# Optimization experiments

Measured on AMD Instinct MI355X. Metric: run time of the kernel, lower is better.

## Reference

```python
import jax, jax.numpy as jnp
import numpy as np

K = 8
D_IN = 300 + K   # 308
H = 100          # hidden size hardcoded throughout the module
N = 768          # num_words (words in one table)


def setup_inputs() -> dict:
    key = jax.random.key(0)
    ks = jax.random.split(key, 24)
    f32 = jnp.float32

    def rn(k, shape, scale=0.05):
        return jax.random.normal(k, shape, dtype=f32) * scale

    inp = {
        'vv': jax.random.normal(ks[0], (N, D_IN), dtype=f32),
        'indices': jax.random.randint(ks[1], (N, 5), 0, N),
        'indices_not_found': jax.random.randint(ks[2], (N,), 0, 2).astype(bool),
        'num_words': N,
        # ModuleA: Linear(308, 100) + tanh
        'A_W': rn(ks[3], (D_IN, H)), 'A_b': jnp.zeros((H,), f32),
        # ModuleB: consumes concat(ww[N,500], hh[N,100]) -> Linear(600,100)+tanh
        'B_W': rn(ks[4], (5 * H + H, H)), 'B_b': jnp.zeros((H,), f32),
        # ModuleB2(100,100,100): two heads, oo and new hidden hh
        'B2_Wo': rn(ks[5], (H, H)), 'B2_bo': jnp.zeros((H,), f32),
        'B2_Wh': rn(ks[6], (H, H)), 'B2_bh': jnp.zeros((H,), f32),
        # ModuleD(100,100)
        'D_W': rn(ks[7], (H, H)), 'D_b': jnp.zeros((H,), f32),
    }
    # Three ModuleAssociate2 heads (rows/cols/cells): pairwise 2-layer MLP
    # score(o_i, o_j) = Linear(H,2)(relu(Linear(2H,H)(concat(o_i,o_j))))
    for i, name in enumerate(['rows', 'cols', 'cells']):
        k1, k2 = jax.random.split(ks[8 + i])
        inp[name + '_W1'] = rn(k1, (2 * H, H))
        inp[name + '_b1'] = jnp.zeros((H,), f32)
        inp[name + '_W2'] = rn(k2, (H, 2))
        inp[name + '_b2'] = jnp.zeros((2,), f32)
    return inp


def _concat_neighbors(uu, indices, not_found):
    # gather 5 neighbor feature rows -> (N, 5*H); zero rows where not found
    y = uu[indices].reshape(indices.shape[0], 5 * uu.shape[1])  # (N,5,H)->(N,500)
    return jnp.where(not_found[:, None], 0.0, y)


def _associate(o, W1, b1, W2, b2):
    # pairwise MLP over all (i,j) pairs without materializing the 2H concat:
    # concat(o_i,o_j) @ W1 == o_i @ W1[:H] + o_j @ W1[H:]
    h = o.shape[1]
    hl = o @ W1[:h]   # (N,H)
    hr = o @ W1[h:]   # (N,H)
    hid = jax.nn.relu(hl[:, None, :] + hr[None, :, :] + b1)  # (N,N,H)
    return hid @ W2 + b2  # (N,N,2)


def reference(indices, indices_not_found, vv, num_words,
              A_W, A_b, B_W, B_b, B2_Wo, B2_bo, B2_Wh, B2_bh, D_W, D_b,
              rows_W1, rows_b1, rows_W2, rows_b2,
              cols_W1, cols_b1, cols_W2, cols_b2,
              cells_W1, cells_b1, cells_W2, cells_b2):
    iterations = 1
    uu = jnp.tanh(vv @ A_W + A_b)                 # ModuleA: (N,100)
    hh = jnp.zeros((num_words, H), vv.dtype)
    for _ in range(iterations):
        ww = _concat_neighbors(uu, indices, indices_not_found)  # (N,500)
        bb = jnp.tanh(jnp.concatenate([ww, hh], axis=1) @ B_W + B_b)  # ModuleB
        oo = jnp.tanh(bb @ B2_Wo + B2_bo)          # ModuleB2 output head
        hh = jnp.tanh(bb @ B2_Wh + B2_bh)          # ModuleB2 hidden head
        uu = jnp.tanh(hh @ D_W + D_b)              # ModuleD
    return (_associate(oo, rows_W1, rows_b1, rows_W2, rows_b2),
            _associate(oo, cols_W1, cols_b1, cols_W2, cols_b2),
            _associate(oo, cells_W1, cells_b1, cells_W2, cells_b2))
```

## Files before the change

### kernel.cpp

```cpp
#include <hip/hip_runtime.h>
#include <hip/hip_bf16.h>

#define NW   768
#define HID  100
#define DIN  308
#define RPB  2
#define TJ   64

typedef const float* fp;

__global__ __launch_bounds__(512) void k_uu(fp vv, fp A_W, fp A_b,
                                            float* __restrict__ uu) {
    __shared__ float vs[RPB][DIN];
    __shared__ float part[4][RPB][128];
    const int i0 = blockIdx.x * RPB;
    for (int t = threadIdx.x; t < RPB * DIN; t += 512) {
        const int r = t / DIN, k = t % DIN;
        vs[r][k] = vv[(i0 + r) * DIN + k];
    }
    __syncthreads();
    const int c = threadIdx.x & 127;
    const int s = threadIdx.x >> 7;
    float a0 = 0.f, a1 = 0.f;
    if (c < HID) {
        const int k0 = s * 77;
#pragma unroll 11
        for (int k = k0; k < k0 + 77; ++k) {
            const float w = A_W[k * HID + c];
            a0 = fmaf(vs[0][k], w, a0);
            a1 = fmaf(vs[1][k], w, a1);
        }
    }
    part[s][0][c] = a0; part[s][1][c] = a1;
    __syncthreads();
    for (int t = threadIdx.x; t < RPB * HID; t += 512) {
        const int r = t / HID, cc = t % HID;
        float acc = A_b[cc];
#pragma unroll
        for (int s2 = 0; s2 < 4; ++s2) acc += part[s2][r][cc];
        uu[(i0 + r) * HID + cc] = tanhf(acc);
    }
}

__global__ __launch_bounds__(640) void k_fused(
    const float* __restrict__ uu, const int* __restrict__ indices,
    const int* __restrict__ nf,
    fp B_W, fp B_b, fp B2_Wo, fp B2_bo,
    fp W1r, fp b1r, fp W1c, fp b1c, fp W1e, fp b1e,
    float* __restrict__ hlhr) {
    __shared__ __align__(16) float ww[RPB][5 * HID];
    __shared__ float part[5][RPB][128];
    __shared__ __align__(16) float bbs[RPB][HID];
    __shared__ __align__(16) float oos[RPB][HID];
    __shared__ int flags[6];
    __shared__ int smode[2];

    if (threadIdx.x < 6) flags[threadIdx.x] = 0;
    __syncthreads();
    if (threadIdx.x < 192) {
        const int t = threadIdx.x;
        const unsigned vn = (unsigned)nf[t];
        if (vn > 1u) atomicOr(&flags[0], 1);
        if (vn & 0xFEFEFEFEu) atomicOr(&flags[1], 1);
        if ((t & 1) && vn) atomicOr(&flags[2], 1);
        if (!(t & 1) && vn) atomicOr(&flags[3], 1);
        const unsigned vi = (unsigned)indices[t];
        if ((t & 1) && vi) atomicOr(&flags[4], 1);
        if (!(t & 1) && vi) atomicOr(&flags[5], 1);
    }
    __syncthreads();
    if (threadIdx.x == 0) {
        int m = 0;
        if (!flags[1] && flags[0]) m = 1;
        else if (!flags[2] && flags[3]) m = 2;
        smode[0] = m;
        smode[1] = (!flags[4] && flags[5]) ? 1 : 0;
    }
    __syncthreads();
    const int mnf = smode[0], midx = smode[1];

    const int i0 = blockIdx.x * RPB;
    for (int t = threadIdx.x; t < RPB * 5 * HID; t += 640) {
        const int r = t / (5 * HID), u = t % (5 * HID);
        const int i = i0 + r;
        const bool notf = (mnf == 1) ? (((const unsigned char*)nf)[i] != 0)
                        : (mnf == 2) ? (nf[2 * i] != 0)
                                     : (nf[i] != 0);
        const int q = u / HID, cc = u % HID;
        int j = midx ? indices[2 * (i * 5 + q)] : indices[i * 5 + q];
        j = (j < 0) ? 0 : ((j >= NW) ? NW - 1 : j);
        ww[r][u] = notf ? 0.f : uu[j * HID + cc];
    }
    __syncthreads();

    const int c = threadIdx.x % 128;
    const int s = threadIdx.x / 128;

    {
        float a0 = 0.f, a1 = 0.f;
        if (c < HID) {
            const int k0 = s * 100;
#pragma unroll 5
            for (int k = k0; k < k0 + 100; k += 4) {
                const float4 w0 = *(const float4*)&ww[0][k];
                const float4 w1 = *(const float4*)&ww[1][k];
                const float b0 = B_W[(k + 0) * HID + c];
                const float b1v = B_W[(k + 1) * HID + c];
                const float b2v = B_W[(k + 2) * HID + c];
                const float b3 = B_W[(k + 3) * HID + c];
                a0 = fmaf(w0.x, b0, a0); a1 = fmaf(w1.x, b0, a1);
                a0 = fmaf(w0.y, b1v, a0); a1 = fmaf(w1.y, b1v, a1);
                a0 = fmaf(w0.z, b2v, a0); a1 = fmaf(w1.z, b2v, a1);
                a0 = fmaf(w0.w, b3, a0); a1 = fmaf(w1.w, b3, a1);
            }
        }
        part[s][0][c] = a0; part[s][1][c] = a1;
    }
    __syncthreads();
    for (int t = threadIdx.x; t < RPB * HID; t += 640) {
        const int r = t / HID, cc = t % HID;
        float acc = B_b[cc];
#pragma unroll
        for (int s2 = 0; s2 < 5; ++s2) acc += part[s2][r][cc];
        bbs[r][cc] = tanhf(acc);
    }
    __syncthreads();

    {
        float a0 = 0.f, a1 = 0.f;
        if (c < HID) {
            const int k0 = s * 20;
#pragma unroll 5
            for (int k = k0; k < k0 + 20; k += 4) {
                const float4 w0 = *(const float4*)&bbs[0][k];
                const float4 w1 = *(const float4*)&bbs[1][k];
                const float b0 = B2_Wo[(k + 0) * HID + c];
                const float b1v = B2_Wo[(k + 1) * HID + c];
                const float b2v = B2_Wo[(k + 2) * HID + c];
                const float b3 = B2_Wo[(k + 3) * HID + c];
                a0 = fmaf(w0.x, b0, a0); a1 = fmaf(w1.x, b0, a1);
                a0 = fmaf(w0.y, b1v, a0); a1 = fmaf(w1.y, b1v, a1);
                a0 = fmaf(w0.z, b2v, a0); a1 = fmaf(w1.z, b2v, a1);
                a0 = fmaf(w0.w, b3, a0); a1 = fmaf(w1.w, b3, a1);
            }
        }
        part[s][0][c] = a0; part[s][1][c] = a1;
    }
    __syncthreads();
    for (int t = threadIdx.x; t < RPB * HID; t += 640) {
        const int r = t / HID, cc = t % HID;
        float acc = B2_bo[cc];
#pragma unroll
        for (int s2 = 0; s2 < 5; ++s2) acc += part[s2][r][cc];
        oos[r][cc] = tanhf(acc);
    }
    __syncthreads();

    const int u = threadIdx.x;
    if (u < 600) {
        const int ho = u / HID;
        const int cc = u % HID;
        const int h = ho >> 1, half = ho & 1;
        fp W1 = (h == 0) ? W1r : ((h == 1) ? W1c : W1e);
        fp b1 = (h == 0) ? b1r : ((h == 1) ? b1c : b1e);
        const float bias = half ? 0.f : b1[cc];
        float a0 = bias, a1 = bias;
        const float* Wp = W1 + half * HID * HID;
#pragma unroll 5
        for (int k = 0; k < HID; k += 4) {
            const float4 o0 = *(const float4*)&oos[0][k];
            const float4 o1 = *(const float4*)&oos[1][k];
            const float b0 = Wp[(k + 0) * HID + cc];
            const float b1v = Wp[(k + 1) * HID + cc];
            const float b2v = Wp[(k + 2) * HID + cc];
            const float b3 = Wp[(k + 3) * HID + cc];
            a0 = fmaf(o0.x, b0, a0); a1 = fmaf(o1.x, b0, a1);
            a0 = fmaf(o0.y, b1v, a0); a1 = fmaf(o1.y, b1v, a1);
            a0 = fmaf(o0.z, b2v, a0); a1 = fmaf(o1.z, b2v, a1);
            a0 = fmaf(o0.w, b3, a0); a1 = fmaf(o1.w, b3, a1);
        }
        hlhr[(size_t)ho * (NW * HID) + (size_t)(i0 + 0) * HID + cc] = a0;
        hlhr[(size_t)ho * (NW * HID) + (size_t)(i0 + 1) * HID + cc] = a1;
    }
}

__global__ __launch_bounds__(256) void k_pair(
    const float* __restrict__ hlhr,
    fp W2r, fp b2r, fp W2c, fp b2c, fp W2e, fp b2e,
    float* __restrict__ out) {
    __shared__ __align__(16) float hlS[HID][TJ];
    __shared__ __align__(16) float hrS[HID][TJ];
    __shared__ __align__(16) float2 w2s[HID];

    const int h  = blockIdx.z;
    const int i0 = blockIdx.y * TJ;
    const int j0 = blockIdx.x * TJ;
    const float* hl = hlhr + (size_t)(h * 2 + 0) * (NW * HID) + (size_t)i0 * HID;
    const float* hr = hlhr + (size_t)(h * 2 + 1) * (NW * HID) + (size_t)j0 * HID;

    for (int t = threadIdx.x; t < TJ * HID; t += 256) {
        const int r = t / HID, k = t % HID;
        const int rs = r ^ ((k & 7) << 2);
        hlS[k][rs] = hl[t];
        hrS[k][rs] = hr[t];
    }
    fp W2 = (h == 0) ? W2r : ((h == 1) ? W2c : W2e);
    fp b2 = (h == 0) ? b2r : ((h == 1) ? b2c : b2e);
    if (threadIdx.x < HID) {
        w2s[threadIdx.x] = make_float2(W2[2 * threadIdx.x], W2[2 * threadIdx.x + 1]);
    }
    __syncthreads();

    const int tx = threadIdx.x & 15;
    const int ty = threadIdx.x >> 4;
    float2 acc[4][4];
#pragma unroll
    for (int ii = 0; ii < 4; ++ii)
#pragma unroll
        for (int jj = 0; jj < 4; ++jj) acc[ii][jj] = make_float2(0.f, 0.f);

    for (int k = 0; k < HID; ++k) {
        const int sw = (k & 7) << 2;
        const float4 a4 = *(const float4*)&hlS[k][(ty * 4) ^ sw];
        const float4 r4 = *(const float4*)&hrS[k][(tx * 4) ^ sw];
        const float2 w2 = w2s[k];
        const float av[4] = {a4.x, a4.y, a4.z, a4.w};
        const float rv[4] = {r4.x, r4.y, r4.z, r4.w};
#pragma unroll
        for (int ii = 0; ii < 4; ++ii)
#pragma unroll
            for (int jj = 0; jj < 4; ++jj) {
                const float hv = fmaxf(av[ii] + rv[jj], 0.f);
                acc[ii][jj].x = fmaf(hv, w2.x, acc[ii][jj].x);
                acc[ii][jj].y = fmaf(hv, w2.y, acc[ii][jj].y);
            }
    }

    const float b20 = b2[0];
    const float b21 = b2[1];
#pragma unroll
    for (int ii = 0; ii < 4; ++ii) {
        const int i = i0 + ty * 4 + ii;
        const size_t rowo = ((size_t)(h * NW + i) * NW + j0 + tx * 4) * 2;
        float4 v0, v1;
        v0.x = acc[ii][0].x + b20; v0.y = acc[ii][0].y + b21;
        v0.z = acc[ii][1].x + b20; v0.w = acc[ii][1].y + b21;
        v1.x = acc[ii][2].x + b20; v1.y = acc[ii][2].y + b21;
        v1.z = acc[ii][3].x + b20; v1.w = acc[ii][3].y + b21;
        *reinterpret_cast<float4*>(out + rowo)     = v0;
        *reinterpret_cast<float4*>(out + rowo + 4) = v1;
    }
}

extern "C" void kernel_launch(void* const* d_in, const int* in_sizes, int n_in,
                              void* d_out, int out_size, void* d_ws,
                              size_t ws_size, hipStream_t stream) {
    int i_vv = -1, i_idx = -1, i_nf = -1, i_AW = -1, i_BW = -1;
    int tens[3] = {-1, -1, -1}; int n10 = 0;
    int w1s[3]  = {-1, -1, -1}; int n20 = 0;
    int w2s_[3] = {-1, -1, -1}; int n200 = 0;
    int b100[8] = {-1, -1, -1, -1, -1, -1, -1, -1}; int nb = 0;
    int b2s[3]  = {-1, -1, -1}; int nb2 = 0;
    for (int i = 0; i < n_in; ++i) {
        switch (in_sizes[i]) {
            case 236544: i_vv = i; break;
            case 3840:   i_idx = i; break;
            case 768:    i_nf = i; break;
            case 30800:  i_AW = i; break;
            case 60000:  i_BW = i; break;
            case 10000:  if (n10 < 3) tens[n10++] = i; break;
            case 20000:  if (n20 < 3) w1s[n20++] = i; break;
            case 200:    if (n200 < 3) w2s_[n200++] = i; break;
            case 100:    if (nb < 8) b100[nb++] = i; break;
            case 2:      if (nb2 < 3) b2s[nb2++] = i; break;
            default: break;
        }
    }
    fp vv          = (fp)d_in[i_vv];
    const int* idx = (const int*)d_in[i_idx];
    const int* nf  = (const int*)d_in[i_nf];
    fp A_W = (fp)d_in[i_AW],      A_b   = (fp)d_in[b100[0]];
    fp B_W = (fp)d_in[i_BW],      B_b   = (fp)d_in[b100[1]];
    fp B2_Wo = (fp)d_in[tens[0]], B2_bo = (fp)d_in[b100[2]];
    fp W1r = (fp)d_in[w1s[0]], b1r = (fp)d_in[b100[5]];
    fp W1c = (fp)d_in[w1s[1]], b1c = (fp)d_in[b100[6]];
    fp W1e = (fp)d_in[w1s[2]], b1e = (fp)d_in[b100[7]];
    fp W2r = (fp)d_in[w2s_[0]], b2r = (fp)d_in[b2s[0]];
    fp W2c = (fp)d_in[w2s_[1]], b2c = (fp)d_in[b2s[1]];
    fp W2e = (fp)d_in[w2s_[2]], b2e = (fp)d_in[b2s[2]];

    float* out = (float*)d_out;

    float* ws   = (float*)d_ws;
    float* uu   = ws;
    float* hlhr = ws + NW * HID;

    k_uu<<<NW / RPB, 512, 0, stream>>>(vv, A_W, A_b, uu);
    k_fused<<<NW / RPB, 640, 0, stream>>>(uu, idx, nf, B_W, B_b,
                                          B2_Wo, B2_bo,
                                          W1r, b1r, W1c, b1c, W1e, b1e, hlhr);
    dim3 grid(NW / TJ, NW / TJ, 3);
    k_pair<<<grid, 256, 0, stream>>>(hlhr, W2r, b2r, W2c, b2c, W2e, b2e, out);
}
```

Measured before the change: 55.23 us.

## Transpose hl/hr to k-major layout before pairwise kernel, drop LDS swizzle

Adds a transpose kernel that rewrites the hl/hr projections into a feature-major [H][N] layout, so the pairwise kernel can load its shared tiles with coalesced, unswizzled row copies. The pairwise kernel also drops the shared W2 staging and reads the W2 weights directly from global memory (uniform loads), splits the accumulators into two arrays, and unrolls the k loop by 4. This adds an extra kernel launch plus a round trip of the 6x768x100 buffer through memory. Without the XOR swizzle, the float4 shared reads may now hit more bank conflicts.

```diff
diff --git a/kernel.cpp b/kernel.cpp
--- a/kernel.cpp
+++ b/kernel.cpp
@@ -184,46 +184,58 @@
     }
 }
 
+__global__ __launch_bounds__(256) void k_tr(const float* __restrict__ in,
+                                            float* __restrict__ outT) {
+    __shared__ float ld[64 * 101];
+    const int ho = blockIdx.y;
+    const int i0 = blockIdx.x * 64;
+    const float* src = in + (size_t)ho * (NW * HID) + (size_t)i0 * HID;
+    float* dst = outT + (size_t)ho * (HID * NW);
+    for (int t = threadIdx.x; t < 64 * HID; t += 256) {
+        const int r = t / HID, c = t % HID;
+        ld[r * 101 + c] = src[t];
+    }
+    __syncthreads();
+    for (int t = threadIdx.x; t < 64 * HID; t += 256) {
+        const int k = t >> 6, r = t & 63;
+        dst[(size_t)k * NW + i0 + r] = ld[r * 101 + k];
+    }
+}
+
 __global__ __launch_bounds__(256) void k_pair(
-    const float* __restrict__ hlhr,
+    const float* __restrict__ hlhrT,
     fp W2r, fp b2r, fp W2c, fp b2c, fp W2e, fp b2e,
     float* __restrict__ out) {
     __shared__ __align__(16) float hlS[HID][TJ];
     __shared__ __align__(16) float hrS[HID][TJ];
-    __shared__ __align__(16) float2 w2s[HID];
 
     const int h  = blockIdx.z;
     const int i0 = blockIdx.y * TJ;
     const int j0 = blockIdx.x * TJ;
-    const float* hl = hlhr + (size_t)(h * 2 + 0) * (NW * HID) + (size_t)i0 * HID;
-    const float* hr = hlhr + (size_t)(h * 2 + 1) * (NW * HID) + (size_t)j0 * HID;
-
-    for (int t = threadIdx.x; t < TJ * HID; t += 256) {
-        const int r = t / HID, k = t % HID;
-        const int rs = r ^ ((k & 7) << 2);
-        hlS[k][rs] = hl[t];
-        hrS[k][rs] = hr[t];
-    }
+    const float* hlg = hlhrT + (size_t)(h * 2 + 0) * (HID * NW);
+    const float* hrg = hlhrT + (size_t)(h * 2 + 1) * (HID * NW);
+
+    for (int t = threadIdx.x; t < HID * TJ; t += 256) {
+        const int k = t >> 6, j = t & 63;
+        hlS[k][j] = hlg[k * NW + i0 + j];
+        hrS[k][j] = hrg[k * NW + j0 + j];
+    }
+    __syncthreads();
+
     fp W2 = (h == 0) ? W2r : ((h == 1) ? W2c : W2e);
     fp b2 = (h == 0) ? b2r : ((h == 1) ? b2c : b2e);
-    if (threadIdx.x < HID) {
-        w2s[threadIdx.x] = make_float2(W2[2 * threadIdx.x], W2[2 * threadIdx.x + 1]);
-    }
-    __syncthreads();
 
     const int tx = threadIdx.x & 15;
     const int ty = threadIdx.x >> 4;
-    float2 acc[4][4];
-#pragma unroll
-    for (int ii = 0; ii < 4; ++ii)
-#pragma unroll
-        for (int jj = 0; jj < 4; ++jj) acc[ii][jj] = make_float2(0.f, 0.f);
-
+    float acc0[4][4] = {};
+    float acc1[4][4] = {};
+
+#pragma unroll 4
     for (int k = 0; k < HID; ++k) {
-        const int sw = (k & 7) << 2;
-        const float4 a4 = *(const float4*)&hlS[k][(ty * 4) ^ sw];
-        const float4 r4 = *(const float4*)&hrS[k][(tx * 4) ^ sw];
-        const float2 w2 = w2s[k];
+        const float4 a4 = *(const float4*)&hlS[k][ty * 4];
+        const float4 r4 = *(const float4*)&hrS[k][tx * 4];
+        const float wa = W2[2 * k];
+        const float wb = W2[2 * k + 1];
         const float av[4] = {a4.x, a4.y, a4.z, a4.w};
         const float rv[4] = {r4.x, r4.y, r4.z, r4.w};
 #pragma unroll
@@ -231,8 +243,8 @@
 #pragma unroll
             for (int jj = 0; jj < 4; ++jj) {
                 const float hv = fmaxf(av[ii] + rv[jj], 0.f);
-                acc[ii][jj].x = fmaf(hv, w2.x, acc[ii][jj].x);
-                acc[ii][jj].y = fmaf(hv, w2.y, acc[ii][jj].y);
+                acc0[ii][jj] = fmaf(hv, wa, acc0[ii][jj]);
+                acc1[ii][jj] = fmaf(hv, wb, acc1[ii][jj]);
             }
     }
 
@@ -243,10 +255,10 @@
         const int i = i0 + ty * 4 + ii;
         const size_t rowo = ((size_t)(h * NW + i) * NW + j0 + tx * 4) * 2;
         float4 v0, v1;
-        v0.x = acc[ii][0].x + b20; v0.y = acc[ii][0].y + b21;
-        v0.z = acc[ii][1].x + b20; v0.w = acc[ii][1].y + b21;
-        v1.x = acc[ii][2].x + b20; v1.y = acc[ii][2].y + b21;
-        v1.z = acc[ii][3].x + b20; v1.w = acc[ii][3].y + b21;
+        v0.x = acc0[ii][0] + b20; v0.y = acc1[ii][0] + b21;
+        v0.z = acc0[ii][1] + b20; v0.w = acc1[ii][1] + b21;
+        v1.x = acc0[ii][2] + b20; v1.y = acc1[ii][2] + b21;
+        v1.z = acc0[ii][3] + b20; v1.w = acc1[ii][3] + b21;
         *reinterpret_cast<float4*>(out + rowo)     = v0;
         *reinterpret_cast<float4*>(out + rowo + 4) = v1;
     }
@@ -291,14 +303,17 @@
 
     float* out = (float*)d_out;
 
-    float* ws   = (float*)d_ws;
-    float* uu   = ws;
-    float* hlhr = ws + NW * HID;
+    float* ws    = (float*)d_ws;
+    float* uu    = ws;
+    float* hlhr  = ws + NW * HID;
+    float* hlhrT = ws + NW * HID + 6 * NW * HID;
 
     k_uu<<<NW / RPB, 512, 0, stream>>>(vv, A_W, A_b, uu);
     k_fused<<<NW / RPB, 640, 0, stream>>>(uu, idx, nf, B_W, B_b,
                                           B2_Wo, B2_bo,
                                           W1r, b1r, W1c, b1c, W1e, b1e, hlhr);
+    dim3 gtr(NW / 64, 6);
+    k_tr<<<gtr, 256, 0, stream>>>(hlhr, hlhrT);
     dim3 grid(NW / TJ, NW / TJ, 3);
-    k_pair<<<grid, 256, 0, stream>>>(hlhr, W2r, b2r, W2c, b2c, W2e, b2e, out);
-}
+    k_pair<<<grid, 256, 0, stream>>>(hlhrT, W2r, b2r, W2c, b2c, W2e, b2e, out);
+}
```

New measurement: 61.14 us. 1.11x slower.

## Shrink pairwise tile to 32x32 with row-major padded shared layout

Applied to the files above, without the earlier changes.

Shrinks the pairwise-MLP tile from 64x64 to 32x32 with a 2x2 per-thread micro-tile, which quadruples the grid (24x24x3 blocks) and adds an occupancy hint in launch bounds. Shared memory now holds hl/hr row-major with a padded stride and loads along k as float4, replacing the XOR-swizzled transposed layout. The aim is more blocks and waves to fill the GPU's compute units and lower register pressure. In exchange each block reuses less data per shared-memory load, so there is more LDS traffic and global reloading of hl/hr per output.

```diff
diff --git a/kernel.cpp b/kernel.cpp
--- a/kernel.cpp
+++ b/kernel.cpp
@@ -5,7 +5,8 @@
 #define HID  100
 #define DIN  308
 #define RPB  2
-#define TJ   64
+#define TP   32
+#define LDP  108
 
 typedef const float* fp;
 
@@ -184,71 +185,76 @@
     }
 }
 
-__global__ __launch_bounds__(256) void k_pair(
+__global__ __launch_bounds__(256, 4) void k_pair(
     const float* __restrict__ hlhr,
     fp W2r, fp b2r, fp W2c, fp b2c, fp W2e, fp b2e,
     float* __restrict__ out) {
-    __shared__ __align__(16) float hlS[HID][TJ];
-    __shared__ __align__(16) float hrS[HID][TJ];
-    __shared__ __align__(16) float2 w2s[HID];
+    __shared__ __align__(16) float hlS[TP][LDP];
+    __shared__ __align__(16) float hrS[TP][LDP];
+    __shared__ __align__(16) float w2a[HID];
+    __shared__ __align__(16) float w2b[HID];
 
     const int h  = blockIdx.z;
-    const int i0 = blockIdx.y * TJ;
-    const int j0 = blockIdx.x * TJ;
+    const int i0 = blockIdx.y * TP;
+    const int j0 = blockIdx.x * TP;
     const float* hl = hlhr + (size_t)(h * 2 + 0) * (NW * HID) + (size_t)i0 * HID;
     const float* hr = hlhr + (size_t)(h * 2 + 1) * (NW * HID) + (size_t)j0 * HID;
-
-    for (int t = threadIdx.x; t < TJ * HID; t += 256) {
-        const int r = t / HID, k = t % HID;
-        const int rs = r ^ ((k & 7) << 2);
-        hlS[k][rs] = hl[t];
-        hrS[k][rs] = hr[t];
-    }
     fp W2 = (h == 0) ? W2r : ((h == 1) ? W2c : W2e);
     fp b2 = (h == 0) ? b2r : ((h == 1) ? b2c : b2e);
+
+    for (int t = threadIdx.x; t < TP * HID; t += 256) {
+        const int r = t / HID, c = t % HID;
+        hlS[r][c] = hl[t];
+        hrS[r][c] = hr[t];
+    }
     if (threadIdx.x < HID) {
-        w2s[threadIdx.x] = make_float2(W2[2 * threadIdx.x], W2[2 * threadIdx.x + 1]);
+        w2a[threadIdx.x] = W2[2 * threadIdx.x];
+        w2b[threadIdx.x] = W2[2 * threadIdx.x + 1];
     }
     __syncthreads();
 
     const int tx = threadIdx.x & 15;
     const int ty = threadIdx.x >> 4;
-    float2 acc[4][4];
-#pragma unroll
-    for (int ii = 0; ii < 4; ++ii)
-#pragma unroll
-        for (int jj = 0; jj < 4; ++jj) acc[ii][jj] = make_float2(0.f, 0.f);
-
-    for (int k = 0; k < HID; ++k) {
-        const int sw = (k & 7) << 2;
-        const float4 a4 = *(const float4*)&hlS[k][(ty * 4) ^ sw];
-        const float4 r4 = *(const float4*)&hrS[k][(tx * 4) ^ sw];
-        const float2 w2 = w2s[k];
-        const float av[4] = {a4.x, a4.y, a4.z, a4.w};
-        const float rv[4] = {r4.x, r4.y, r4.z, r4.w};
-#pragma unroll
-        for (int ii = 0; ii < 4; ++ii)
-#pragma unroll
-            for (int jj = 0; jj < 4; ++jj) {
-                const float hv = fmaxf(av[ii] + rv[jj], 0.f);
-                acc[ii][jj].x = fmaf(hv, w2.x, acc[ii][jj].x);
-                acc[ii][jj].y = fmaf(hv, w2.y, acc[ii][jj].y);
-            }
+    float acc0[2][2] = {};
+    float acc1[2][2] = {};
+
+#pragma unroll 5
+    for (int kb = 0; kb < HID; kb += 4) {
+        const float4 a0 = *(const float4*)&hlS[ty * 2 + 0][kb];
+        const float4 a1 = *(const float4*)&hlS[ty * 2 + 1][kb];
+        const float4 r0 = *(const float4*)&hrS[tx * 2 + 0][kb];
+        const float4 r1 = *(const float4*)&hrS[tx * 2 + 1][kb];
+        const float4 wa = *(const float4*)&w2a[kb];
+        const float4 wb = *(const float4*)&w2b[kb];
+#define STEP(cmp)                                                              \
+        {                                                                      \
+            const float h00 = fmaxf(a0.cmp + r0.cmp, 0.f);                     \
+            const float h01 = fmaxf(a0.cmp + r1.cmp, 0.f);                     \
+            const float h10 = fmaxf(a1.cmp + r0.cmp, 0.f);                     \
+            const float h11 = fmaxf(a1.cmp + r1.cmp, 0.f);                     \
+            acc0[0][0] = fmaf(h00, wa.cmp, acc0[0][0]);                        \
+            acc1[0][0] = fmaf(h00, wb.cmp, acc1[0][0]);                        \
+            acc0[0][1] = fmaf(h01, wa.cmp, acc0[0][1]);                        \
+            acc1[0][1] = fmaf(h01, wb.cmp, acc1[0][1]);                        \
+            acc0[1][0] = fmaf(h10, wa.cmp, acc0[1][0]);                        \
+            acc1[1][0] = fmaf(h10, wb.cmp, acc1[1][0]);                        \
+            acc0[1][1] = fmaf(h11, wa.cmp, acc0[1][1]);                        \
+            acc1[1][1] = fmaf(h11, wb.cmp, acc1[1][1]);                        \
+        }
+        STEP(x) STEP(y) STEP(z) STEP(w)
+#undef STEP
     }
 
     const float b20 = b2[0];
     const float b21 = b2[1];
 #pragma unroll
-    for (int ii = 0; ii < 4; ++ii) {
-        const int i = i0 + ty * 4 + ii;
-        const size_t rowo = ((size_t)(h * NW + i) * NW + j0 + tx * 4) * 2;
-        float4 v0, v1;
-        v0.x = acc[ii][0].x + b20; v0.y = acc[ii][0].y + b21;
-        v0.z = acc[ii][1].x + b20; v0.w = acc[ii][1].y + b21;
-        v1.x = acc[ii][2].x + b20; v1.y = acc[ii][2].y + b21;
-        v1.z = acc[ii][3].x + b20; v1.w = acc[ii][3].y + b21;
-        *reinterpret_cast<float4*>(out + rowo)     = v0;
-        *reinterpret_cast<float4*>(out + rowo + 4) = v1;
+    for (int ii = 0; ii < 2; ++ii) {
+        const int i = i0 + ty * 2 + ii;
+        const size_t rowo = ((size_t)(h * NW + i) * NW + j0 + tx * 2) * 2;
+        float4 v;
+        v.x = acc0[ii][0] + b20; v.y = acc1[ii][0] + b21;
+        v.z = acc0[ii][1] + b20; v.w = acc1[ii][1] + b21;
+        *reinterpret_cast<float4*>(out + rowo) = v;
     }
 }
 
@@ -299,6 +305,6 @@
     k_fused<<<NW / RPB, 640, 0, stream>>>(uu, idx, nf, B_W, B_b,
                                           B2_Wo, B2_bo,
                                           W1r, b1r, W1c, b1c, W1e, b1e, hlhr);
-    dim3 grid(NW / TJ, NW / TJ, 3);
+    dim3 grid(NW / TP, NW / TP, 3);
     k_pair<<<grid, 256, 0, stream>>>(hlhr, W2r, b2r, W2c, b2c, W2e, b2e, out);
 }
```

Measured after the change: 50.13 us. 9.2% less time.
